# Optimization experiments

Measured on AMD Instinct MI355X. Metric: run time of the kernel, lower is better.

The kernel has to match this reference:

```python
import jax, jax.numpy as jnp
import numpy as np

COMMITMENT_COST = 0.25
NUM_EMBEDDINGS = 512

def _conv(x, w, b=None, stride=1, pad=1):
    y = jax.lax.conv_general_dilated(x, w, (stride, stride), [(pad, pad)] * 2,
                                     dimension_numbers=('NCHW', 'OIHW', 'NCHW'))
    return y if b is None else y + b[None, :, None, None]

def _tconv(x, w, b, stride=2, k=4, p=1):
    # torch ConvTranspose2d(in,out,k,s,p): weight (in,out,kh,kw)
    w2 = jnp.flip(w, (2, 3)).transpose(1, 0, 2, 3)  # -> (out,in,kh,kw)
    pad = k - 1 - p
    y = jax.lax.conv_general_dilated(x, w2, (1, 1), [(pad, pad)] * 2,
                                     lhs_dilation=(stride, stride),
                                     dimension_numbers=('NCHW', 'OIHW', 'NCHW'))
    return y + b[None, :, None, None]

def _residual(x, w1, w2):
    return x + _conv(jax.nn.relu(_conv(jax.nn.relu(x), w1)), w2)

def _res_stack(x, w11, w12, w21, w22):
    x = jax.nn.relu(_residual(x, w11, w12))
    return jax.nn.relu(_residual(x, w21, w22))

def _vq(z, codebook):
    # z: (B, D, H, W) -> NHWC
    inputs = z.transpose(0, 2, 3, 1)
    B, H, W, D = inputs.shape
    flat = inputs.reshape(-1, D)  # (N, D)
    # squared euclidean distances (argmin-equivalent to torch.cdist)
    d2 = (jnp.sum(flat * flat, 1, keepdims=True)
          - 2.0 * flat @ codebook.T
          + jnp.sum(codebook * codebook, 1)[None, :])  # (N, K)
    idx = jnp.argmin(d2, axis=1)
    quantized = codebook[idx].reshape(B, H, W, D)
    sg = jax.lax.stop_gradient
    e_latent_loss = jnp.mean((sg(quantized) - inputs) ** 2)
    q_latent_loss = jnp.mean((quantized - sg(inputs)) ** 2)
    loss = q_latent_loss + COMMITMENT_COST * e_latent_loss
    quantized_st = inputs + sg(quantized - inputs)
    avg_probs = jnp.bincount(idx, length=NUM_EMBEDDINGS).astype(jnp.float32) / flat.shape[0]
    perplexity = jnp.exp(-jnp.sum(avg_probs * jnp.log(avg_probs + 1e-10)))
    return loss, quantized_st.transpose(0, 3, 1, 2), perplexity

def setup_inputs() -> dict:
    key = jax.random.key(0)
    ks = jax.random.split(key, 24)
    Hc, D, K = 128, 64, NUM_EMBEDDINGS
    s = 0.05
    rn = lambda k, sh: (jax.random.normal(k, sh, jnp.float32) * s)
    inp = {
        'x': jax.random.normal(ks[0], (32, 3, 256, 256), jnp.float32),
        # encoder
        'e1w': rn(ks[1], (Hc // 2, 3, 4, 4)), 'e1b': rn(ks[2], (Hc // 2,)),
        'e2w': rn(ks[3], (Hc, Hc // 2, 4, 4)), 'e2b': rn(ks[4], (Hc,)),
        'er11': rn(ks[5], (Hc, Hc, 3, 3)), 'er12': rn(ks[6], (Hc, Hc, 3, 3)),
        'er21': rn(ks[7], (Hc, Hc, 3, 3)), 'er22': rn(ks[8], (Hc, Hc, 3, 3)),
        # pre-vq conv 1x1
        'pvw': rn(ks[9], (D, Hc, 1, 1)), 'pvb': rn(ks[10], (D,)),
        # codebook: uniform(-1/K, 1/K)
        'cb': jax.random.uniform(ks[11], (K, D), jnp.float32, -1.0 / K, 1.0 / K),
        # decoder
        'd1w': rn(ks[12], (Hc, D, 3, 3)), 'd1b': rn(ks[13], (Hc,)),
        'dr11': rn(ks[14], (Hc, Hc, 3, 3)), 'dr12': rn(ks[15], (Hc, Hc, 3, 3)),
        'dr21': rn(ks[16], (Hc, Hc, 3, 3)), 'dr22': rn(ks[17], (Hc, Hc, 3, 3)),
        't1w': rn(ks[18], (Hc, Hc // 2, 4, 4)), 't1b': rn(ks[19], (Hc // 2,)),
        't2w': rn(ks[20], (Hc // 2, 3, 4, 4)), 't2b': rn(ks[21], (3,)),
    }
    return inp

def reference(x, e1w, e1b, e2w, e2b, er11, er12, er21, er22, pvw, pvb, cb,
              d1w, d1b, dr11, dr12, dr21, dr22, t1w, t1b, t2w, t2b):
    # encoder
    z = jax.nn.relu(_conv(x, e1w, e1b, stride=2, pad=1))
    z = _conv(z, e2w, e2b, stride=2, pad=1)
    z = _res_stack(z, er11, er12, er21, er22)
    # pre-vq 1x1 conv
    z = _conv(z, pvw, pvb, stride=1, pad=0)
    # vector quantization
    loss, quantized, perplexity = _vq(z, cb)
    # decoder
    h = _conv(quantized, d1w, d1b, stride=1, pad=1)
    h = _res_stack(h, dr11, dr12, dr21, dr22)
    h = jax.nn.relu(_tconv(h, t1w, t1b))
    x_recon = _tconv(h, t2w, t2b)
    return loss, x_recon, perplexity
```

## Files before the change

### kernel.cpp

```cpp
#include <hip/hip_runtime.h>

typedef short bf16x8 __attribute__((ext_vector_type(8)));
typedef float f32x4 __attribute__((ext_vector_type(4)));
typedef unsigned short ushort4v __attribute__((ext_vector_type(4)));
typedef unsigned int u32x4 __attribute__((ext_vector_type(4)));

__device__ __forceinline__ unsigned short f2bf(float f) {
  unsigned u = __float_as_uint(f);
  unsigned r = (u + 0x7FFFu + ((u >> 16) & 1u)) >> 16;
  return (unsigned short)r;
}
__device__ __forceinline__ float bf2f(unsigned short u) {
  return __uint_as_float(((unsigned)u) << 16);
}

__device__ __forceinline__ bf16x8 relu_bf8(bf16x8 v) {
  u32x4 u;
  __builtin_memcpy(&u, &v, 16);
  #pragma unroll
  for (int i = 0; i < 4; i++) {
    unsigned s = u[i] & 0x80008000u;
    u[i] &= ~((s >> 15) * 0xFFFFu);
  }
  bf16x8 r;
  __builtin_memcpy(&r, &u, 16);
  return r;
}

__device__ __forceinline__ int xcd_swz(int bid, int n) {
  return (bid & 7) * (n >> 3) + (bid >> 3);
}

__global__ void init_k(int* __restrict__ hist) {
  int t = threadIdx.x;
  if (t < 512) hist[t] = 0;
}

__global__ void cbh_k(const float* __restrict__ cb, float* __restrict__ cbh) {
  int k = blockIdx.x * 256 + threadIdx.x;
  if (k >= 512) return;
  const float* c = cb + k * 64;
  float s = 0.f;
  #pragma unroll
  for (int d = 0; d < 64; d++) s = fmaf(c[d], c[d], s);
  cbh[k] = 0.5f * s;
}

__global__ void repack_cbf_k(const float* __restrict__ cb,
                             unsigned short* __restrict__ cbf) {
  int idx = blockIdx.x * 256 + threadIdx.x;
  if (idx >= 32768) return;
  int j = idx & 7;
  int lane = (idx >> 3) & 63;
  int ks = (idx >> 9) & 1;
  int m = idx >> 10;
  int code = m * 16 + (lane & 15);
  int d = ks * 32 + (lane >> 4) * 8 + j;
  cbf[idx] = f2bf(cb[code * 64 + d]);
}

template <int CIN>
__global__ void repack_frag_k(const float* __restrict__ w,
                              unsigned short* __restrict__ wf) {
  int idx = blockIdx.x * 256 + threadIdx.x;
  int total = (CIN / 32) * 9 * 8 * 512;
  if (idx >= total) return;
  int j = idx & 7;
  int lane = (idx >> 3) & 63;
  int M = (idx >> 9) & 7;
  int tk = idx >> 12;
  int tap = tk % 9;
  int kstep = tk / 9;
  int co = M * 16 + (lane & 15);
  int ci = kstep * 32 + (lane >> 4) * 8 + j;
  wf[idx] = f2bf(w[((size_t)co * CIN + ci) * 9 + tap]);
}

__global__ void repack_e2f_k(const float* __restrict__ w,
                             unsigned short* __restrict__ wf) {
  int idx = blockIdx.x * 256 + threadIdx.x;
  if (idx >= 131072) return;
  int j = idx & 7;
  int lane = (idx >> 3) & 63;
  int M = (idx >> 9) & 7;
  int tap = (idx >> 12) & 15;
  int ks = idx >> 16;
  int co = M * 16 + (lane & 15);
  int ci = ks * 32 + (lane >> 4) * 8 + j;
  wf[idx] = f2bf(w[((size_t)co * 64 + ci) * 16 + tap]);
}

__global__ void repack_pvf_k(const float* __restrict__ w,
                             unsigned short* __restrict__ wf) {
  int idx = blockIdx.x * 256 + threadIdx.x;
  if (idx >= 8192) return;
  int j = idx & 7;
  int lane = (idx >> 3) & 63;
  int m = (idx >> 9) & 3;
  int ks = idx >> 11;
  int co = m * 16 + (lane & 15);
  int ci = ks * 32 + (lane >> 4) * 8 + j;
  wf[idx] = f2bf(w[co * 128 + ci]);
}

__global__ void repack_t1f_k(const float* __restrict__ w,
                             unsigned short* __restrict__ wf) {
  int idx = blockIdx.x * 256 + threadIdx.x;
  if (idx >= 131072) return;
  int j = idx & 7;
  int lane = (idx >> 3) & 63;
  int m = (idx >> 9) & 3;
  int tap = (idx >> 11) & 3;
  int ks = (idx >> 13) & 3;
  int par = (idx >> 15) & 3;
  int sy = par >> 1, sx = par & 1;
  int ty = tap >> 1, tx = tap & 1;
  int ky = sy ? (ty ? 0 : 2) : (ty ? 1 : 3);
  int kx = sx ? (tx ? 0 : 2) : (tx ? 1 : 3);
  int co = m * 16 + (lane & 15);
  int ci = ks * 32 + (lane >> 4) * 8 + j;
  wf[idx] = f2bf(w[((size_t)ci * 64 + co) * 16 + ky * 4 + kx]);
}

__global__ void repack_t2f_k(const float* __restrict__ w,
                             unsigned short* __restrict__ wf) {
  int idx = blockIdx.x * 256 + threadIdx.x;
  if (idx >= 16384) return;
  int j = idx & 7;
  int lane = (idx >> 3) & 63;
  int tap = (idx >> 9) & 3;
  int ks = (idx >> 11) & 1;
  int par = idx >> 12;
  int sy = par >> 1, sx = par & 1;
  int ty = tap >> 1, tx = tap & 1;
  int ky = sy ? (ty ? 0 : 2) : (ty ? 1 : 3);
  int kx = sx ? (tx ? 0 : 2) : (tx ? 1 : 3);
  int co = lane & 15;
  int ci = ks * 32 + (lane >> 4) * 8 + j;
  float v = (co < 3) ? w[((size_t)ci * 3 + co) * 16 + ky * 4 + kx] : 0.f;
  wf[idx] = f2bf(v);
}

__global__ __launch_bounds__(256) void e1_k(
    const float* __restrict__ x, const float* __restrict__ w,
    const float* __restrict__ bias, unsigned short* __restrict__ out) {
  int gid = blockIdx.x * 256 + threadIdx.x;
  int b = gid >> 14;
  int rem = gid & 16383;
  int oy = rem >> 7, ox = rem & 127;
  float iv[48];
  const float* xb = x + (size_t)b * 3 * 65536;
  #pragma unroll
  for (int ci = 0; ci < 3; ci++)
    #pragma unroll
    for (int ky = 0; ky < 4; ky++) {
      int iy = 2 * oy - 1 + ky;
      #pragma unroll
      for (int kx = 0; kx < 4; kx++) {
        int ix = 2 * ox - 1 + kx;
        float v = 0.f;
        if ((unsigned)iy < 256u && (unsigned)ix < 256u)
          v = xb[ci * 65536 + iy * 256 + ix];
        iv[ci * 16 + ky * 4 + kx] = v;
      }
    }
  unsigned hw[32];
  for (int cp = 0; cp < 32; cp++) {
    float a0 = bias[2 * cp], a1 = bias[2 * cp + 1];
    const float* w0 = w + (2 * cp) * 48;
    const float* w1 = w0 + 48;
    #pragma unroll
    for (int k = 0; k < 48; k++) {
      a0 = fmaf(iv[k], w0[k], a0);
      a1 = fmaf(iv[k], w1[k], a1);
    }
    hw[cp] = (unsigned)f2bf(fmaxf(a0, 0.f)) |
             ((unsigned)f2bf(fmaxf(a1, 0.f)) << 16);
  }
  u32x4* ob = (u32x4*)(out + ((size_t)b * 16384 + oy * 128 + ox) * 64);
  #pragma unroll
  for (int g = 0; g < 8; g++)
    ob[g] = (u32x4){hw[4 * g], hw[4 * g + 1], hw[4 * g + 2], hw[4 * g + 3]};
}

__global__ __launch_bounds__(256, 4) void e2m_k(
    const unsigned short* __restrict__ in,
    const unsigned short* __restrict__ wf, const float* __restrict__ bias,
    unsigned short* __restrict__ out) {
  __shared__ unsigned short patch[528 * 36];
  int blk = xcd_swz(blockIdx.x, gridDim.x);
  int b = blk >> 6;
  int oy = blk & 63;
  int t = threadIdx.x;
  int w = t >> 6, l = t & 63;
  int cib = (l >> 4) * 8, colb = l & 15;
  f32x4 acc[2][4];
  #pragma unroll
  for (int m = 0; m < 2; m++)
    #pragma unroll
    for (int n = 0; n < 4; n++) acc[m][n] = (f32x4){0.f, 0.f, 0.f, 0.f};
  const unsigned short* inb = in + (size_t)b * 16384 * 64;
  for (int ks = 0; ks < 2; ks++) {
    __syncthreads();
    for (int idx = t; idx < 2112; idx += 256) {
      int q = idx & 3;
      int pos = idx >> 2;
      int r = pos / 132, c = pos - r * 132;
      int iy = 2 * oy - 1 + r, ix = c - 1;
      bf16x8 v = (bf16x8){0, 0, 0, 0, 0, 0, 0, 0};
      if ((unsigned)iy < 128u && (unsigned)ix < 128u)
        v = *(const bf16x8*)&inb[((size_t)iy * 128 + ix) * 64 + ks * 32 + q * 8];
      int s = (c >> 1) + (c & 1) * 66;
      *(bf16x8*)&patch[(r * 132 + s) * 36 + q * 8] = v;
    }
    __syncthreads();
    __builtin_amdgcn_s_setprio(1);
    #pragma unroll
    for (int tap = 0; tap < 16; tap++) {
      int ky = tap >> 2, kx = tap & 3;
      bf16x8 bfrag[4];
      #pragma unroll
      for (int n = 0; n < 4; n++) {
        int ox = n * 16 + colb;
        int pos = ky * 132 + (kx & 1) * 66 + ox + (kx >> 1);
        bfrag[n] = *(const bf16x8*)&patch[pos * 36 + cib];
      }
      const unsigned short* wft = wf + ((size_t)(ks * 16 + tap) * 8) * 512;
      #pragma unroll
      for (int m = 0; m < 2; m++) {
        bf16x8 af = *(const bf16x8*)&wft[((w * 2 + m) * 64 + l) * 8];
        #pragma unroll
        for (int n = 0; n < 4; n++)
          acc[m][n] = __builtin_amdgcn_mfma_f32_16x16x32_bf16(af, bfrag[n],
                                                              acc[m][n], 0, 0, 0);
      }
    }
    __builtin_amdgcn_s_setprio(0);
  }
  #pragma unroll
  for (int m = 0; m < 2; m++) {
    int cob = (w * 2 + m) * 16 + (l >> 4) * 4;
    f32x4 bj = *(const f32x4*)&bias[cob];
    #pragma unroll
    for (int n = 0; n < 4; n++) {
      int ox = n * 16 + colb;
      size_t adr = ((size_t)(b * 4096 + oy * 64 + ox)) * 128 + cob;
      ushort4v pre = {f2bf(acc[m][n][0] + bj[0]), f2bf(acc[m][n][1] + bj[1]),
                      f2bf(acc[m][n][2] + bj[2]), f2bf(acc[m][n][3] + bj[3])};
      *(ushort4v*)&out[adr] = pre;
    }
  }
}

template <int CIN, bool RES_ADD, bool RELU_IN, bool HAS_BIAS, bool PRE_ONLY>
__global__ __launch_bounds__(256, 4) void conv3nh_k(
    const unsigned short* __restrict__ in,
    const unsigned short* __restrict__ wf,
    const float* __restrict__ bias,
    const unsigned short* __restrict__ res,
    unsigned short* __restrict__ out) {
  constexpr int KSTEPS = CIN / 32;
  __shared__ unsigned short patch[264 * 40];
  int blk = xcd_swz(blockIdx.x, gridDim.x);
  int b = blk >> 5;
  int tile = blk & 31;
  int y0 = tile * 2;
  int t = threadIdx.x;
  int w = t >> 6, l = t & 63;
  int wm = w >> 1, wn = w & 1;
  int n0 = wn * 64;
  int cib = (l >> 4) * 8, colb = l & 15;
  f32x4 acc[4][4];
  #pragma unroll
  for (int m = 0; m < 4; m++)
    #pragma unroll
    for (int n = 0; n < 4; n++) acc[m][n] = (f32x4){0.f, 0.f, 0.f, 0.f};
  const unsigned short* inb = in + (size_t)b * 4096 * CIN;
  for (int ks = 0; ks < KSTEPS; ks++) {
    __syncthreads();
    for (int idx = t; idx < 1056; idx += 256) {
      int q = idx & 3;
      int pos = idx >> 2;
      int r = pos / 66, c = pos - r * 66;
      int y = y0 - 1 + r, x = c - 1;
      bf16x8 v = (bf16x8){0, 0, 0, 0, 0, 0, 0, 0};
      if ((unsigned)y < 64u && (unsigned)x < 64u)
        v = *(const bf16x8*)&inb[((size_t)(y * 64 + x)) * CIN + ks * 32 + q * 8];
      if (RELU_IN) v = relu_bf8(v);
      *(bf16x8*)&patch[pos * 40 + q * 8] = v;
    }
    __syncthreads();
    __builtin_amdgcn_s_setprio(1);
    const unsigned short* wfk = wf + (size_t)ks * 9 * 4096;
    #pragma unroll
    for (int tap = 0; tap < 9; tap++) {
      int ky = tap / 3, kx = tap % 3;
      bf16x8 bfrag[4];
      #pragma unroll
      for (int n = 0; n < 4; n++) {
        int p = n0 + n * 16 + colb;
        int pr = p >> 6, pc = p & 63;
        int pos = (pr + ky) * 66 + (pc + kx);
        bfrag[n] = *(const bf16x8*)&patch[pos * 40 + cib];
      }
      const unsigned short* wft = wfk + tap * 4096;
      bf16x8 afrag[4];
      #pragma unroll
      for (int m = 0; m < 4; m++)
        afrag[m] = *(const bf16x8*)&wft[((wm * 4 + m) * 64 + l) * 8];
      #pragma unroll
      for (int m = 0; m < 4; m++)
        #pragma unroll
        for (int n = 0; n < 4; n++)
          acc[m][n] = __builtin_amdgcn_mfma_f32_16x16x32_bf16(
              afrag[m], bfrag[n], acc[m][n], 0, 0, 0);
    }
    __builtin_amdgcn_s_setprio(0);
  }
  #pragma unroll
  for (int m = 0; m < 4; m++) {
    int cobase = wm * 64 + m * 16 + (l >> 4) * 4;
    float b0 = HAS_BIAS ? bias[cobase] : 0.f;
    float b1 = HAS_BIAS ? bias[cobase + 1] : 0.f;
    float b2 = HAS_BIAS ? bias[cobase + 2] : 0.f;
    float b3 = HAS_BIAS ? bias[cobase + 3] : 0.f;
    #pragma unroll
    for (int n = 0; n < 4; n++) {
      int p = n0 + n * 16 + colb;
      size_t adr = ((size_t)(b * 4096 + tile * 128 + p)) * 128 + cobase;
      float f0 = acc[m][n][0] + b0, f1 = acc[m][n][1] + b1;
      float f2 = acc[m][n][2] + b2, f3 = acc[m][n][3] + b3;
      if (RES_ADD) {
        ushort4v rv = *(const ushort4v*)&res[adr];
        f0 += bf2f(rv.x); f1 += bf2f(rv.y); f2 += bf2f(rv.z); f3 += bf2f(rv.w);
      }
      ushort4v pk;
      if (PRE_ONLY) {
        pk.x = f2bf(f0); pk.y = f2bf(f1); pk.z = f2bf(f2); pk.w = f2bf(f3);
      } else {
        pk.x = f2bf(fmaxf(f0, 0.f)); pk.y = f2bf(fmaxf(f1, 0.f));
        pk.z = f2bf(fmaxf(f2, 0.f)); pk.w = f2bf(fmaxf(f3, 0.f));
      }
      *(ushort4v*)&out[adr] = pk;
    }
  }
}

__global__ __launch_bounds__(256, 4) void pvqm_k(
    const unsigned short* __restrict__ in,
    const unsigned short* __restrict__ wf, const float* __restrict__ bias,
    unsigned short* __restrict__ z) {
  int blk = blockIdx.x;
  int b = blk >> 4;
  int hw0 = (blk & 15) * 256;
  int t = threadIdx.x;
  int w = t >> 6, l = t & 63;
  int n0 = w * 64;
  int cib = (l >> 4) * 8, colb = l & 15;
  f32x4 acc[4][4];
  #pragma unroll
  for (int m = 0; m < 4; m++)
    #pragma unroll
    for (int n = 0; n < 4; n++) acc[m][n] = (f32x4){0.f, 0.f, 0.f, 0.f};
  const unsigned short* inb = in + ((size_t)(b * 4096 + hw0)) * 128;
  for (int ks = 0; ks < 4; ks++) {
    bf16x8 bfrag[4];
    #pragma unroll
    for (int n = 0; n < 4; n++) {
      int p = n0 + n * 16 + colb;
      bfrag[n] = *(const bf16x8*)&inb[(size_t)p * 128 + ks * 32 + cib];
    }
    const unsigned short* wk = wf + ks * 4 * 512;
    #pragma unroll
    for (int m = 0; m < 4; m++) {
      bf16x8 af = *(const bf16x8*)&wk[(m * 64 + l) * 8];
      #pragma unroll
      for (int n = 0; n < 4; n++)
        acc[m][n] = __builtin_amdgcn_mfma_f32_16x16x32_bf16(af, bfrag[n],
                                                            acc[m][n], 0, 0, 0);
    }
  }
  #pragma unroll
  for (int m = 0; m < 4; m++) {
    int cob = m * 16 + (l >> 4) * 4;
    f32x4 bj = *(const f32x4*)&bias[cob];
    #pragma unroll
    for (int n = 0; n < 4; n++) {
      int p = n0 + n * 16 + colb;
      ushort4v pk = {f2bf(acc[m][n][0] + bj[0]), f2bf(acc[m][n][1] + bj[1]),
                     f2bf(acc[m][n][2] + bj[2]), f2bf(acc[m][n][3] + bj[3])};
      *(ushort4v*)&z[((size_t)(b * 4096 + hw0 + p)) * 64 + cob] = pk;
    }
  }
}

__global__ __launch_bounds__(256, 2) void vq_argmin_k(
    const unsigned short* __restrict__ z,
    const unsigned short* __restrict__ cbf, const float* __restrict__ cbh,
    unsigned short* __restrict__ bidx) {
  __shared__ unsigned short bidx_s[256];
  int blk = blockIdx.x;
  int b = blk >> 4;
  int hw0 = (blk & 15) * 256;
  int t = threadIdx.x;
  int w = t >> 6, l = t & 63;
  int colb = l & 15, cib = (l >> 4) * 8;
  const unsigned short* zb = z + ((size_t)(b * 4096 + hw0)) * 64;
  bf16x8 bfrag[4][2];
  #pragma unroll
  for (int n = 0; n < 4; n++) {
    int p = w * 64 + n * 16 + colb;
    #pragma unroll
    for (int ks = 0; ks < 2; ks++)
      bfrag[n][ks] = *(const bf16x8*)&zb[(size_t)p * 64 + ks * 32 + cib];
  }
  float best[4];
  int bid[4];
  #pragma unroll
  for (int n = 0; n < 4; n++) { best[n] = -1e30f; bid[n] = 0; }
  for (int m = 0; m < 32; m++) {
    bf16x8 a0 = *(const bf16x8*)&cbf[((size_t)(m * 2 + 0) * 64 + l) * 8];
    bf16x8 a1 = *(const bf16x8*)&cbf[((size_t)(m * 2 + 1) * 64 + l) * 8];
    int code0 = m * 16 + (l >> 4) * 4;
    f32x4 ch = *(const f32x4*)&cbh[code0];
    #pragma unroll
    for (int n = 0; n < 4; n++) {
      f32x4 acc = (f32x4){0.f, 0.f, 0.f, 0.f};
      acc = __builtin_amdgcn_mfma_f32_16x16x32_bf16(a0, bfrag[n][0], acc, 0, 0, 0);
      acc = __builtin_amdgcn_mfma_f32_16x16x32_bf16(a1, bfrag[n][1], acc, 0, 0, 0);
      #pragma unroll
      for (int r = 0; r < 4; r++) {
        float sc = acc[r] - ch[r];
        if (sc > best[n]) { best[n] = sc; bid[n] = code0 + r; }
      }
    }
  }
  #pragma unroll
  for (int n = 0; n < 4; n++) {
    #pragma unroll
    for (int off = 16; off <= 32; off <<= 1) {
      float ob = __shfl_xor(best[n], off, 64);
      int oi = __shfl_xor(bid[n], off, 64);
      if (ob > best[n] || (ob == best[n] && oi < bid[n])) {
        best[n] = ob;
        bid[n] = oi;
      }
    }
    if ((l >> 4) == 0) bidx_s[w * 64 + n * 16 + colb] = (unsigned short)bid[n];
  }
  __syncthreads();
  bidx[(size_t)b * 4096 + hw0 + t] = bidx_s[t];
}

__global__ __launch_bounds__(256, 4) void vq_apply_k(
    const unsigned short* __restrict__ z,
    const float* __restrict__ cb, const unsigned short* __restrict__ bidx,
    unsigned short* __restrict__ q,
    float* __restrict__ part, int part_off) {
  __shared__ float red[256];
  int blk = blockIdx.x;
  int t = threadIdx.x;
  size_t pxg = (size_t)blk * 256 + t;
  int bi = bidx[pxg];
  const float* cq = cb + bi * 64;
  const unsigned short* zp = z + pxg * 64;
  unsigned short* qp = q + pxg * 64;
  float ls = 0.f;
  #pragma unroll
  for (int g = 0; g < 8; g++) {
    u32x4 zv = *(const u32x4*)&zp[g * 8];
    u32x4 qv;
    #pragma unroll
    for (int h = 0; h < 4; h++) {
      int d = g * 8 + h * 2;
      float q0 = cq[d], q1 = cq[d + 1];
      float z0 = __uint_as_float(zv[h] << 16);
      float z1 = __uint_as_float(zv[h] & 0xFFFF0000u);
      float d0 = q0 - z0, d1 = q1 - z1;
      ls = fmaf(d0, d0, ls);
      ls = fmaf(d1, d1, ls);
      qv[h] = (unsigned)f2bf(q0) | ((unsigned)f2bf(q1) << 16);
    }
    *(u32x4*)&qp[g * 8] = qv;
  }
  red[t] = ls;
  __syncthreads();
  for (int s = 128; s > 0; s >>= 1) {
    if (t < s) red[t] += red[t + s];
    __syncthreads();
  }
  if (t == 0) part[part_off + blk] = red[0];
}

__global__ __launch_bounds__(1024) void vq_hist_k(
    const unsigned short* __restrict__ bidx, int* __restrict__ hist) {
  __shared__ int hl[512];
  int t = threadIdx.x;
  if (t < 512) hl[t] = 0;
  __syncthreads();
  int base = blockIdx.x * 16384;
  for (int i = t; i < 16384; i += 1024)
    atomicAdd(&hl[bidx[base + i]], 1);
  __syncthreads();
  if (t < 512 && hl[t] > 0) atomicAdd(&hist[t], hl[t]);
}

__global__ __launch_bounds__(256, 2) void t1m_k(
    const unsigned short* __restrict__ in,
    const unsigned short* __restrict__ wf, const float* __restrict__ bias,
    unsigned short* __restrict__ out) {
  __shared__ unsigned short patch[264 * 40];
  int blk = xcd_swz(blockIdx.x, gridDim.x);
  int b = blk >> 5;
  int a0 = (blk & 31) * 2;
  int t = threadIdx.x;
  int w = t >> 6, l = t & 63;
  int sy = w >> 1, sx = w & 1;
  int cib = (l >> 4) * 8, colb = l & 15;
  f32x4 acc[4][8];
  #pragma unroll
  for (int m = 0; m < 4; m++)
    #pragma unroll
    for (int n = 0; n < 8; n++) acc[m][n] = (f32x4){0.f, 0.f, 0.f, 0.f};
  const unsigned short* inb = in + (size_t)b * 4096 * 128;
  for (int ks = 0; ks < 4; ks++) {
    __syncthreads();
    for (int idx = t; idx < 1056; idx += 256) {
      int q = idx & 3;
      int pos = idx >> 2;
      int r = pos / 66, c = pos - r * 66;
      int y = a0 - 1 + r, x = c - 1;
      bf16x8 v = (bf16x8){0, 0, 0, 0, 0, 0, 0, 0};
      if ((unsigned)y < 64u && (unsigned)x < 64u)
        v = *(const bf16x8*)&inb[((size_t)(y * 64 + x)) * 128 + ks * 32 + q * 8];
      *(bf16x8*)&patch[pos * 40 + q * 8] = v;
    }
    __syncthreads();
    __builtin_amdgcn_s_setprio(1);
    const unsigned short* wpar = wf + (size_t)((sy * 2 + sx) * 4 + ks) * 8192;
    #pragma unroll
    for (int tap = 0; tap < 4; tap++) {
      int ty = tap >> 1, tx = tap & 1;
      int d = sy ? ty + 1 : ty;
      int e = sx ? tx + 1 : tx;
      bf16x8 bfrag[8];
      #pragma unroll
      for (int n = 0; n < 8; n++) {
        int p = n * 16 + colb;
        int ar = p >> 6, pc = p & 63;
        int pos = (ar + d) * 66 + (pc + e);
        bfrag[n] = *(const bf16x8*)&patch[pos * 40 + cib];
      }
      bf16x8 afrag[4];
      #pragma unroll
      for (int m = 0; m < 4; m++)
        afrag[m] = *(const bf16x8*)&wpar[(tap * 256 + m * 64 + l) * 8];
      #pragma unroll
      for (int m = 0; m < 4; m++)
        #pragma unroll
        for (int n = 0; n < 8; n++)
          acc[m][n] = __builtin_amdgcn_mfma_f32_16x16x32_bf16(
              afrag[m], bfrag[n], acc[m][n], 0, 0, 0);
    }
    __builtin_amdgcn_s_setprio(0);
  }
  #pragma unroll
  for (int m = 0; m < 4; m++) {
    int cob = m * 16 + (l >> 4) * 4;
    float b0 = bias[cob], b1 = bias[cob + 1], b2 = bias[cob + 2],
          b3 = bias[cob + 3];
    #pragma unroll
    for (int n = 0; n < 8; n++) {
      int p = n * 16 + colb;
      int ar = p >> 6, pc = p & 63;
      int oy = 2 * (a0 + ar) + sy, ox = 2 * pc + sx;
      ushort4v pk;
      pk.x = f2bf(fmaxf(acc[m][n][0] + b0, 0.f));
      pk.y = f2bf(fmaxf(acc[m][n][1] + b1, 0.f));
      pk.z = f2bf(fmaxf(acc[m][n][2] + b2, 0.f));
      pk.w = f2bf(fmaxf(acc[m][n][3] + b3, 0.f));
      *(ushort4v*)&out[((size_t)b * 16384 + oy * 128 + ox) * 64 + cob] = pk;
    }
  }
}

__global__ __launch_bounds__(256, 2) void t2m_k(
    const unsigned short* __restrict__ in,
    const unsigned short* __restrict__ wf,
    const float* __restrict__ bias, float* __restrict__ out) {
  __shared__ unsigned short patch[528 * 40];
  int blk = xcd_swz(blockIdx.x, gridDim.x);
  int b = blk >> 6;
  int a0 = (blk & 63) * 2;
  int t = threadIdx.x;
  int w = t >> 6, l = t & 63;
  int sy = w >> 1, sx = w & 1;
  int cib = (l >> 4) * 8, colb = l & 15;
  f32x4 acc[2][8];
  #pragma unroll
  for (int ar = 0; ar < 2; ar++)
    #pragma unroll
    for (int n = 0; n < 8; n++) acc[ar][n] = (f32x4){0.f, 0.f, 0.f, 0.f};
  bf16x8 af[2][4];
  #pragma unroll
  for (int ks = 0; ks < 2; ks++) {
    const unsigned short* wpar = wf + (size_t)((sy * 2 + sx) * 2 + ks) * 2048;
    #pragma unroll
    for (int tap = 0; tap < 4; tap++)
      af[ks][tap] = *(const bf16x8*)&wpar[(tap * 64 + l) * 8];
  }
  const unsigned short* inb = in + (size_t)b * 16384 * 64;
  for (int ks = 0; ks < 2; ks++) {
    __syncthreads();
    for (int idx = t; idx < 2112; idx += 256) {
      int q = idx & 3;
      int pos = idx >> 2;
      int r = pos / 132, c = pos - r * 132;
      int y = a0 - 1 + r, x = c - 1;
      bf16x8 v = (bf16x8){0, 0, 0, 0, 0, 0, 0, 0};
      if ((unsigned)y < 128u && (unsigned)x < 128u)
        v = *(const bf16x8*)&inb[((size_t)(y * 128 + x)) * 64 + ks * 32 + q * 8];
      *(bf16x8*)&patch[pos * 40 + q * 8] = v;
    }
    __syncthreads();
    __builtin_amdgcn_s_setprio(1);
    #pragma unroll
    for (int tap = 0; tap < 4; tap++) {
      int ty = tap >> 1, tx = tap & 1;
      int d = sy ? ty + 1 : ty;
      int e = sx ? tx + 1 : tx;
      #pragma unroll
      for (int ar = 0; ar < 2; ar++) {
        #pragma unroll
        for (int n = 0; n < 8; n++) {
          int pc = n * 16 + colb;
          int pos = (ar + d) * 132 + (pc + e);
          bf16x8 bfrag = *(const bf16x8*)&patch[pos * 40 + cib];
          acc[ar][n] = __builtin_amdgcn_mfma_f32_16x16x32_bf16(
              af[ks][tap], bfrag, acc[ar][n], 0, 0, 0);
        }
      }
    }
    __builtin_amdgcn_s_setprio(0);
  }
  int rb = (l >> 4) * 4;
  #pragma unroll
  for (int r = 0; r < 4; r++) {
    int co = rb + r;
    if (co < 3) {
      float bj = bias[co];
      #pragma unroll
      for (int ar = 0; ar < 2; ar++) {
        int oy = 2 * (a0 + ar) + sy;
        #pragma unroll
        for (int n = 0; n < 8; n++) {
          int pc = n * 16 + colb;
          int ox = 2 * pc + sx;
          out[((size_t)(b * 3 + co)) * 65536 + oy * 256 + ox] = acc[ar][n][r] + bj;
        }
      }
    }
  }
}

__global__ __launch_bounds__(512) void fin_k(
    const float* __restrict__ part, const int* __restrict__ hist,
    float* __restrict__ loss_out, float* __restrict__ perp_out) {
  __shared__ float red[512];
  int t = threadIdx.x;
  red[t] = part[t];
  __syncthreads();
  for (int s = 256; s > 0; s >>= 1) {
    if (t < s) red[t] += red[t + s];
    __syncthreads();
  }
  float loss = 1.25f * red[0] / 8388608.f;
  __syncthreads();
  float p = (float)hist[t] / 131072.f;
  red[t] = -p * logf(p + 1e-10f);
  __syncthreads();
  for (int s = 256; s > 0; s >>= 1) {
    if (t < s) red[t] += red[t + s];
    __syncthreads();
  }
  if (t == 0) {
    *loss_out = loss;
    *perp_out = expf(red[0]);
  }
}

extern "C" void kernel_launch(void* const* d_in, const int* in_sizes, int n_in,
                              void* d_out, int out_size, void* d_ws, size_t ws_size,
                              hipStream_t stream) {
  (void)in_sizes; (void)n_in; (void)out_size;
  const float* x    = (const float*)d_in[0];
  const float* e1w  = (const float*)d_in[1];
  const float* e1b  = (const float*)d_in[2];
  const float* e2w  = (const float*)d_in[3];
  const float* e2b  = (const float*)d_in[4];
  const float* er11 = (const float*)d_in[5];
  const float* er12 = (const float*)d_in[6];
  const float* er21 = (const float*)d_in[7];
  const float* er22 = (const float*)d_in[8];
  const float* pvw  = (const float*)d_in[9];
  const float* pvb  = (const float*)d_in[10];
  const float* cb   = (const float*)d_in[11];
  const float* d1w  = (const float*)d_in[12];
  const float* d1b  = (const float*)d_in[13];
  const float* dr11 = (const float*)d_in[14];
  const float* dr12 = (const float*)d_in[15];
  const float* dr21 = (const float*)d_in[16];
  const float* dr22 = (const float*)d_in[17];
  const float* t1w  = (const float*)d_in[18];
  const float* t1b  = (const float*)d_in[19];
  const float* t2w  = (const float*)d_in[20];
  const float* t2b  = (const float*)d_in[21];
  float* out = (float*)d_out;

  const size_t W_PVF  = 0;
  const size_t W_E2F  = W_PVF + 4096;
  const size_t W_T1F  = W_E2F + 65536;
  const size_t W_T2F  = W_T1F + 65536;
  const size_t W_D1F  = W_T2F + 8192;
  const size_t W_CBF  = W_D1F + 36864;
  const size_t W_RT   = W_CBF + 16384;
  const size_t W_CBH  = W_RT + 8 * 73728;
  const size_t W_PART = W_CBH + 512;
  const size_t W_BIDX = W_PART + 512;
  const size_t W_HIST = W_BIDX + 65536;
  const size_t W_TOT  = W_HIST + 512;

  float* ws = (float*)d_ws;
  unsigned short* pvf = (unsigned short*)(ws + W_PVF);
  unsigned short* e2f = (unsigned short*)(ws + W_E2F);
  unsigned short* t1f = (unsigned short*)(ws + W_T1F);
  unsigned short* t2f = (unsigned short*)(ws + W_T2F);
  unsigned short* d1f = (unsigned short*)(ws + W_D1F);
  unsigned short* cbf = (unsigned short*)(ws + W_CBF);
  unsigned short* rtf[8];
  for (int i = 0; i < 8; i++)
    rtf[i] = (unsigned short*)(ws + W_RT + (size_t)i * 73728);
  float* cbh  = ws + W_CBH;
  float* part = ws + W_PART;
  unsigned short* bidx = (unsigned short*)(ws + W_BIDX);
  int*   hist = (int*)(ws + W_HIST);

  size_t wfloats = ws_size / sizeof(float);
  int BC = 32;
  while (BC > 1 && W_TOT + (size_t)BC * 1572864 > wfloats) BC >>= 1;
  int nchunk = 32 / BC;

  unsigned short* E1  = (unsigned short*)(ws + W_TOT);
  unsigned short* P1  = (unsigned short*)(ws + W_TOT + (size_t)BC * 524288);
  unsigned short* P2  = P1 + (size_t)BC * 524288;
  unsigned short* P4  = P2 + (size_t)BC * 524288;
  unsigned short* Zbf = P4 + (size_t)BC * 524288;
  unsigned short* Qbf = Zbf + (size_t)BC * 262144;

  init_k<<<1, 512, 0, stream>>>(hist);
  cbh_k<<<2, 256, 0, stream>>>(cb, cbh);
  repack_cbf_k<<<128, 256, 0, stream>>>(cb, cbf);

  repack_pvf_k<<<32, 256, 0, stream>>>(pvw, pvf);
  repack_e2f_k<<<512, 256, 0, stream>>>(e2w, e2f);
  repack_t1f_k<<<512, 256, 0, stream>>>(t1w, t1f);
  repack_t2f_k<<<64, 256, 0, stream>>>(t2w, t2f);
  repack_frag_k<64><<<288, 256, 0, stream>>>(d1w, d1f);
  repack_frag_k<128><<<576, 256, 0, stream>>>(er11, rtf[0]);
  repack_frag_k<128><<<576, 256, 0, stream>>>(er12, rtf[1]);
  repack_frag_k<128><<<576, 256, 0, stream>>>(er21, rtf[2]);
  repack_frag_k<128><<<576, 256, 0, stream>>>(er22, rtf[3]);
  repack_frag_k<128><<<576, 256, 0, stream>>>(dr11, rtf[4]);
  repack_frag_k<128><<<576, 256, 0, stream>>>(dr12, rtf[5]);
  repack_frag_k<128><<<576, 256, 0, stream>>>(dr21, rtf[6]);
  repack_frag_k<128><<<576, 256, 0, stream>>>(dr22, rtf[7]);

  for (int c = 0; c < nchunk; ++c) {
    const float* xc = x + (size_t)c * BC * 3 * 65536;
    float* outc = out + 1 + (size_t)c * BC * 3 * 65536;
    unsigned short* bidxc = bidx + (size_t)c * BC * 4096;
    e1_k<<<BC * 64, 256, 0, stream>>>(xc, e1w, e1b, E1);
    e2m_k<<<BC * 64, 256, 0, stream>>>(E1, e2f, e2b, P1);
    conv3nh_k<128, false, true,  false, false><<<BC * 32, 256, 0, stream>>>(P1, rtf[0], nullptr, nullptr, P4);
    conv3nh_k<128, true,  false, false, false><<<BC * 32, 256, 0, stream>>>(P4, rtf[1], nullptr, P1, P2);
    conv3nh_k<128, false, false, false, false><<<BC * 32, 256, 0, stream>>>(P2, rtf[2], nullptr, nullptr, P4);
    conv3nh_k<128, true,  false, false, false><<<BC * 32, 256, 0, stream>>>(P4, rtf[3], nullptr, P2, P1);
    pvqm_k<<<BC * 16, 256, 0, stream>>>(P1, pvf, pvb, Zbf);
    vq_argmin_k<<<BC * 16, 256, 0, stream>>>(Zbf, cbf, cbh, bidxc);
    vq_apply_k<<<BC * 16, 256, 0, stream>>>(Zbf, cb, bidxc, Qbf, part, c * BC * 16);
    conv3nh_k<64,  false, false, true,  true ><<<BC * 32, 256, 0, stream>>>(Qbf, d1f, d1b, nullptr, P1);
    conv3nh_k<128, false, true,  false, false><<<BC * 32, 256, 0, stream>>>(P1, rtf[4], nullptr, nullptr, P4);
    conv3nh_k<128, true,  false, false, false><<<BC * 32, 256, 0, stream>>>(P4, rtf[5], nullptr, P1, P2);
    conv3nh_k<128, false, false, false, false><<<BC * 32, 256, 0, stream>>>(P2, rtf[6], nullptr, nullptr, P4);
    conv3nh_k<128, true,  false, false, false><<<BC * 32, 256, 0, stream>>>(P4, rtf[7], nullptr, P2, P1);
    t1m_k<<<BC * 32, 256, 0, stream>>>(P1, t1f, t1b, E1);
    t2m_k<<<BC * 64, 256, 0, stream>>>(E1, t2f, t2b, outc);
  }
  vq_hist_k<<<8, 1024, 0, stream>>>(bidx, hist);
  fin_k<<<1, 512, 0, stream>>>(part, hist, out, out + 1 + 6291456);
}
```

Measured before the change: 675.1 us.

## Rewrite first encoder conv as bf16 MFMA im2col kernel

After: 650.1 us. -3.7%, faster.

```diff
diff --git a/kernel.cpp b/kernel.cpp
--- a/kernel.cpp
+++ b/kernel.cpp
@@ -74,6 +74,20 @@
   int co = M * 16 + (lane & 15);
   int ci = kstep * 32 + (lane >> 4) * 8 + j;
   wf[idx] = f2bf(w[((size_t)co * CIN + ci) * 9 + tap]);
+}
+
+__global__ void repack_e1f_k(const float* __restrict__ w,
+                             unsigned short* __restrict__ wf) {
+  int idx = blockIdx.x * 256 + threadIdx.x;
+  if (idx >= 4096) return;
+  int j = idx & 7;
+  int lane = (idx >> 3) & 63;
+  int m = (idx >> 9) & 3;
+  int ks = idx >> 11;
+  int co = m * 16 + (lane & 15);
+  int k = ks * 32 + (lane >> 4) * 8 + j;
+  float v = (k < 48) ? w[co * 48 + k] : 0.f;
+  wf[idx] = f2bf(v);
 }
 
 __global__ void repack_e2f_k(const float* __restrict__ w,
@@ -141,46 +155,70 @@
   wf[idx] = f2bf(v);
 }
 
-__global__ __launch_bounds__(256) void e1_k(
-    const float* __restrict__ x, const float* __restrict__ w,
+__global__ __launch_bounds__(256, 4) void e1m_k(
+    const float* __restrict__ x, const unsigned short* __restrict__ wf,
     const float* __restrict__ bias, unsigned short* __restrict__ out) {
-  int gid = blockIdx.x * 256 + threadIdx.x;
-  int b = gid >> 14;
-  int rem = gid & 16383;
-  int oy = rem >> 7, ox = rem & 127;
-  float iv[48];
+  __shared__ unsigned short patch[128 * 72];
+  int blk = xcd_swz(blockIdx.x, gridDim.x);
+  int b = blk >> 7;
+  int oy = blk & 127;
+  int t = threadIdx.x;
+  int w = t >> 6, l = t & 63;
+  int cib = (l >> 4) * 8, colb = l & 15;
   const float* xb = x + (size_t)b * 3 * 65536;
-  #pragma unroll
-  for (int ci = 0; ci < 3; ci++)
-    #pragma unroll
-    for (int ky = 0; ky < 4; ky++) {
-      int iy = 2 * oy - 1 + ky;
-      #pragma unroll
-      for (int kx = 0; kx < 4; kx++) {
-        int ix = 2 * ox - 1 + kx;
+  {
+    int p = t & 127;
+    int kb = (t >> 7) * 32;
+    int px2 = 2 * p - 1;
+    int oy2 = 2 * oy - 1;
+    bf16x8 pk[4];
+    #pragma unroll
+    for (int c = 0; c < 4; c++) {
+      #pragma unroll
+      for (int j = 0; j < 8; j++) {
+        int k = kb + c * 8 + j;
         float v = 0.f;
-        if ((unsigned)iy < 256u && (unsigned)ix < 256u)
-          v = xb[ci * 65536 + iy * 256 + ix];
-        iv[ci * 16 + ky * 4 + kx] = v;
-      }
-    }
-  unsigned hw[32];
-  for (int cp = 0; cp < 32; cp++) {
-    float a0 = bias[2 * cp], a1 = bias[2 * cp + 1];
-    const float* w0 = w + (2 * cp) * 48;
-    const float* w1 = w0 + 48;
-    #pragma unroll
-    for (int k = 0; k < 48; k++) {
-      a0 = fmaf(iv[k], w0[k], a0);
-      a1 = fmaf(iv[k], w1[k], a1);
-    }
-    hw[cp] = (unsigned)f2bf(fmaxf(a0, 0.f)) |
-             ((unsigned)f2bf(fmaxf(a1, 0.f)) << 16);
-  }
-  u32x4* ob = (u32x4*)(out + ((size_t)b * 16384 + oy * 128 + ox) * 64);
-  #pragma unroll
-  for (int g = 0; g < 8; g++)
-    ob[g] = (u32x4){hw[4 * g], hw[4 * g + 1], hw[4 * g + 2], hw[4 * g + 3]};
+        if (k < 48) {
+          int ci = k >> 4;
+          int ky = (k >> 2) & 3, kx = k & 3;
+          int iy = oy2 + ky, ix = px2 + kx;
+          if ((unsigned)iy < 256u && (unsigned)ix < 256u)
+            v = xb[ci * 65536 + iy * 256 + ix];
+        }
+        pk[c][j] = (short)f2bf(v);
+      }
+    }
+    unsigned short* row = &patch[p * 72 + kb];
+    #pragma unroll
+    for (int c = 0; c < 4; c++)
+      *(bf16x8*)&row[c * 8] = pk[c];
+  }
+  __syncthreads();
+  f32x4 acc[8];
+  #pragma unroll
+  for (int n = 0; n < 8; n++) acc[n] = (f32x4){0.f, 0.f, 0.f, 0.f};
+  #pragma unroll
+  for (int ks = 0; ks < 2; ks++) {
+    bf16x8 af = *(const bf16x8*)&wf[((size_t)(ks * 4 + w) * 64 + l) * 8];
+    #pragma unroll
+    for (int n = 0; n < 8; n++) {
+      bf16x8 bfrag =
+          *(const bf16x8*)&patch[(n * 16 + colb) * 72 + ks * 32 + cib];
+      acc[n] = __builtin_amdgcn_mfma_f32_16x16x32_bf16(af, bfrag, acc[n],
+                                                       0, 0, 0);
+    }
+  }
+  int cob = w * 16 + (l >> 4) * 4;
+  f32x4 bj = *(const f32x4*)&bias[cob];
+  #pragma unroll
+  for (int n = 0; n < 8; n++) {
+    int p = n * 16 + colb;
+    ushort4v pk = {f2bf(fmaxf(acc[n][0] + bj[0], 0.f)),
+                   f2bf(fmaxf(acc[n][1] + bj[1], 0.f)),
+                   f2bf(fmaxf(acc[n][2] + bj[2], 0.f)),
+                   f2bf(fmaxf(acc[n][3] + bj[3], 0.f))};
+    *(ushort4v*)&out[((size_t)b * 16384 + oy * 128 + p) * 64 + cob] = pk;
+  }
 }
 
 __global__ __launch_bounds__(256, 4) void e2m_k(
@@ -723,7 +761,8 @@
   const size_t W_T2F  = W_T1F + 65536;
   const size_t W_D1F  = W_T2F + 8192;
   const size_t W_CBF  = W_D1F + 36864;
-  const size_t W_RT   = W_CBF + 16384;
+  const size_t W_E1F  = W_CBF + 16384;
+  const size_t W_RT   = W_E1F + 2048;
   const size_t W_CBH  = W_RT + 8 * 73728;
   const size_t W_PART = W_CBH + 512;
   const size_t W_BIDX = W_PART + 512;
@@ -737,6 +776,7 @@
   unsigned short* t2f = (unsigned short*)(ws + W_T2F);
   unsigned short* d1f = (unsigned short*)(ws + W_D1F);
   unsigned short* cbf = (unsigned short*)(ws + W_CBF);
+  unsigned short* e1f = (unsigned short*)(ws + W_E1F);
   unsigned short* rtf[8];
   for (int i = 0; i < 8; i++)
     rtf[i] = (unsigned short*)(ws + W_RT + (size_t)i * 73728);
@@ -761,6 +801,7 @@
   cbh_k<<<2, 256, 0, stream>>>(cb, cbh);
   repack_cbf_k<<<128, 256, 0, stream>>>(cb, cbf);
 
+  repack_e1f_k<<<16, 256, 0, stream>>>(e1w, e1f);
   repack_pvf_k<<<32, 256, 0, stream>>>(pvw, pvf);
   repack_e2f_k<<<512, 256, 0, stream>>>(e2w, e2f);
   repack_t1f_k<<<512, 256, 0, stream>>>(t1w, t1f);
@@ -779,7 +820,7 @@
     const float* xc = x + (size_t)c * BC * 3 * 65536;
     float* outc = out + 1 + (size_t)c * BC * 3 * 65536;
     unsigned short* bidxc = bidx + (size_t)c * BC * 4096;
-    e1_k<<<BC * 64, 256, 0, stream>>>(xc, e1w, e1b, E1);
+    e1m_k<<<BC * 128, 256, 0, stream>>>(xc, e1f, e1b, E1);
     e2m_k<<<BC * 64, 256, 0, stream>>>(E1, e2f, e2b, P1);
     conv3nh_k<128, false, true,  false, false><<<BC * 32, 256, 0, stream>>>(P1, rtf[0], nullptr, nullptr, P4);
     conv3nh_k<128, true,  false, false, false><<<BC * 32, 256, 0, stream>>>(P4, rtf[1], nullptr, P1, P2);
```
